# Optimization experiments

Measured on AMD Instinct MI355X. Metric: run time of the kernel, lower is better.

## Reference

```python
import jax, jax.numpy as jnp
import numpy as np

GRID = 32
N = GRID * GRID
KTOP = 256          # max off-diagonal points kept per diagram (rest are diagonal, zero cost)
SINK_ITERS = 150
_idx = np.arange(N).reshape(GRID, GRID)
_EU = np.concatenate([_idx[:, :-1].ravel(), _idx[:-1, :].ravel()]).astype(np.int32)
_EV = np.concatenate([_idx[:, 1:].ravel(), _idx[1:, :].ravel()]).astype(np.int32)
E = _EU.shape[0]  # 1984 grid edges (4-connectivity, V-construction cubical complex)


def _h0_pairs(v):
    """0-dim persistence pairs of the sublevel filtration of pixel values v [N].
    Kruskal/union-find with the elder rule; trivial edges emit diagonal (w, w) pairs."""
    eu, ev = jnp.asarray(_EU), jnp.asarray(_EV)
    w = jnp.maximum(v[eu], v[ev])
    order = jnp.argsort(w)

    @jax.checkpoint
    def step(state, edge):
        parent, birth = state
        u, vv, wgt = edge
        for _ in range(10):              # pointer jumping: full compression (2^10 >= N)
            parent = parent[parent]
        ru, rv = parent[u], parent[vv]
        bu, bv = birth[ru], birth[rv]
        merge = ru != rv
        u_older = bu <= bv
        older = jnp.where(u_older, ru, rv)
        younger = jnp.where(u_older, rv, ru)
        pb = jnp.where(merge, jnp.maximum(bu, bv), wgt)   # younger component dies
        parent = parent.at[younger].set(jnp.where(merge, older, younger))
        birth = birth.at[older].set(jnp.minimum(bu, bv))
        return (parent, birth), (pb, wgt)

    init = (jnp.arange(N, dtype=jnp.int32), v)
    _, (bs, ds) = jax.lax.scan(step, init, (eu[order], ev[order], w[order]))
    return bs, ds


def _diagrams(img):
    """img [GRID,GRID] -> (b0, d0, b1, d1), each [KTOP]. H1 via superlevel H0 duality."""
    v = img.reshape(-1)
    b0, d0 = _h0_pairs(v)
    b0 = jnp.concatenate([b0, v.min()[None]])   # essential H0 class: (min, max)
    d0 = jnp.concatenate([d0, v.max()[None]])
    nb, nd = _h0_pairs(-v)                       # superlevel-set H0 (essential dropped)
    b1, d1 = -nd, -nb

    def topk(b, d):
        _, i = jax.lax.top_k(d - b, KTOP)        # keep most persistent points
        return b[i], d[i]

    return (*topk(b0, d0), *topk(b1, d1))


def _wasserstein(ab, ad, bb, bd):
    """Entropic 1-Wasserstein between diagrams with L-inf ground metric and diagonal slots."""
    K = ab.shape[0]
    Pa = jnp.stack([ab, ad], -1)
    Pb = jnp.stack([bb, bd], -1)
    Mpp = jnp.max(jnp.abs(Pa[:, None, :] - Pb[None, :, :]), -1)  # [K,K]
    da = 0.5 * (ad - ab)                       # L-inf distance of a-points to diagonal
    db = 0.5 * (bd - bb)
    C = jnp.block([[Mpp, jnp.broadcast_to(da[:, None], (K, K))],
                   [jnp.broadcast_to(db[None, :], (K, K)), jnp.zeros((K, K), ab.dtype)]])
    eps = 0.02 * jnp.maximum(jnp.max(C), 1e-6)

    def it(_, fg):
        f, g = fg
        f = -eps * jax.nn.logsumexp((g[None, :] - C) / eps, axis=1)
        g = -eps * jax.nn.logsumexp((f[:, None] - C) / eps, axis=0)
        return f, g

    f, g = jax.lax.fori_loop(0, SINK_ITERS, it, (jnp.zeros(2 * K), jnp.zeros(2 * K)))
    P = jnp.exp((f[:, None] + g[None, :] - C) / eps)
    return jnp.sum(P * C)


def setup_inputs() -> dict:
    key = jax.random.key(0)
    kx, ky = jax.random.split(key)
    x = jax.random.normal(kx, (4, 4, 256, 256), dtype=jnp.float32)
    y = jax.random.randint(ky, (4, 1, 256, 256), 0, 4)
    return {"x": x, "y": y}


def reference(x, y):
    B, C, H, W = x.shape
    x = jax.nn.softmax(x, axis=1)                               # apply_nonlin
    y_oh = (y == jnp.arange(C)[None, :, None, None]).astype(x.dtype)  # scatter_ one-hot
    kh, kw = H // GRID, W // GRID

    def pool(t):  # adaptive_avg_pool2d to (32, 32)
        b, c = t.shape[:2]
        return t.reshape(b, c, GRID, kh, GRID, kw).mean((3, 5))

    mx = pool(x[:, 1:]).reshape(-1, GRID, GRID)  # drop background channel
    my = pool(y_oh[:, 1:]).reshape(-1, GRID, GRID)
    dx = jax.vmap(_diagrams)(mx)
    dy = jax.vmap(_diagrams)(my)
    w0 = jax.vmap(_wasserstein)(dx[0], dx[1], dy[0], dy[1])
    w1 = jax.vmap(_wasserstein)(dx[2], dx[3], dy[2], dy[3])
    return (jnp.sum(w0) + jnp.sum(w1)) / B
```

## Files before the change

kernel.cpp:

```cpp
#include <hip/hip_runtime.h>
#include <cmath>

#define NPIX 1024
#define NEDGE 1984
#define NPAD 2048
#define KTOP 256
#define NITER 150

typedef __attribute__((ext_vector_type(8))) short bf16x8_t;
typedef __attribute__((ext_vector_type(4))) float f32x4_t;

__device__ __forceinline__ unsigned bf_rne(float x) {
    unsigned b = __float_as_uint(x);
    return (b + 0x7fffu + ((b >> 16) & 1u)) >> 16;
}
__device__ __forceinline__ float rcpf(float x) { return __builtin_amdgcn_rcpf(x); }

template<int CTRL>
__device__ __forceinline__ float dppf(float x) {
    return __int_as_float(__builtin_amdgcn_update_dpp(
        __float_as_int(x), __float_as_int(x), CTRL, 0xF, 0xF, false));
}
__device__ __forceinline__ void wave_red2(float& s, float& m) {
    s += dppf<0x121>(s); m = fminf(m, dppf<0x121>(m));
    s += dppf<0x122>(s); m = fminf(m, dppf<0x122>(m));
    s += dppf<0x124>(s); m = fminf(m, dppf<0x124>(m));
    s += dppf<0x128>(s); m = fminf(m, dppf<0x128>(m));
    s += __int_as_float(__builtin_amdgcn_ds_swizzle(__float_as_int(s), 0x401F));
    m = fminf(m, __int_as_float(__builtin_amdgcn_ds_swizzle(__float_as_int(m), 0x401F)));
    float s0 = __int_as_float(__builtin_amdgcn_readlane(__float_as_int(s), 0));
    float s1 = __int_as_float(__builtin_amdgcn_readlane(__float_as_int(s), 32));
    s = s0 + s1;
    float m0 = __int_as_float(__builtin_amdgcn_readlane(__float_as_int(m), 0));
    float m1 = __int_as_float(__builtin_amdgcn_readlane(__float_as_int(m), 32));
    m = fminf(m0, m1);
}

__device__ __forceinline__ float min8v(const float* a) {
    float4 x0 = *(const float4*)a, x1 = *(const float4*)(a + 4);
    return fminf(fminf(fminf(x0.x, x0.y), fminf(x0.z, x0.w)),
                 fminf(fminf(x1.x, x1.y), fminf(x1.z, x1.w)));
}
__device__ __forceinline__ float sum8v(const float* a) {
    float4 x0 = *(const float4*)a, x1 = *(const float4*)(a + 4);
    return ((x0.x + x0.y) + (x0.z + x0.w)) + ((x1.x + x1.y) + (x1.z + x1.w));
}

__global__ __launch_bounds__(256) void pool_kernel(const float* __restrict__ x,
                                                   const int* __restrict__ y,
                                                   float* __restrict__ pooled) {
    int blk = blockIdx.x;
    int img = blk >> 2;
    int cell = ((blk & 3) << 8) | threadIdx.x;
    int gi = cell >> 5, gj = cell & 31;
    const float L2E = 1.4426950408889634f;
    float acc = 0.f;
    if (img < 12) {
        int b = img / 3, c = img % 3 + 1;
        const float* xb = x + (size_t)b * 262144 + (size_t)gi * 2048 + gj * 8;
        for (int pi = 0; pi < 8; ++pi) {
            const float* xr = xb + pi * 256;
            #pragma unroll
            for (int ph = 0; ph < 2; ++ph) {
                float4 c0 = *(const float4*)(xr + ph * 4);
                float4 c1 = *(const float4*)(xr + ph * 4 + 65536);
                float4 c2 = *(const float4*)(xr + ph * 4 + 131072);
                float4 c3 = *(const float4*)(xr + ph * 4 + 196608);
                const float* f0 = (const float*)&c0;
                const float* f1 = (const float*)&c1;
                const float* f2 = (const float*)&c2;
                const float* f3 = (const float*)&c3;
                #pragma unroll
                for (int k = 0; k < 4; ++k) {
                    float e0 = exp2f(f0[k] * L2E), e1 = exp2f(f1[k] * L2E);
                    float e2 = exp2f(f2[k] * L2E), e3 = exp2f(f3[k] * L2E);
                    float ec = (c == 1) ? e1 : (c == 2) ? e2 : e3;
                    acc += ec / (e0 + e1 + e2 + e3);
                }
            }
        }
    } else {
        int tt = img - 12;
        int b = tt / 3, c = tt % 3 + 1;
        const int* yb = y + (size_t)b * 65536 + (size_t)gi * 2048 + gj * 8;
        int cnt = 0;
        for (int pi = 0; pi < 8; ++pi) {
            const int* yr = yb + pi * 256;
            #pragma unroll
            for (int pj = 0; pj < 8; ++pj) cnt += (yr[pj] == c) ? 1 : 0;
        }
        acc = (float)cnt;
    }
    pooled[img * NPIX + cell] = acc * (1.f / 64.f);
}

__device__ void bitonic2048(unsigned long long* keys, int tid, bool asc) {
    for (int k = 2; k <= NPAD; k <<= 1) {
        for (int j = k >> 1; j > 0; j >>= 1) {
            for (int ii = tid; ii < NPAD; ii += 512) {
                int l = ii ^ j;
                if (l > ii) {
                    unsigned long long a = keys[ii], b = keys[l];
                    bool up = (((ii & k) == 0) == asc);
                    if ((a > b) == up) { keys[ii] = b; keys[l] = a; }
                }
            }
            __syncthreads();
        }
    }
}

__global__ __launch_bounds__(512) void diag_kernel(const float* __restrict__ pooled,
                                                   float* __restrict__ diag) {
    __shared__ float v_[NPIX];
    __shared__ unsigned long long keys[NPAD];
    __shared__ unsigned long long PB[NPIX];
    __shared__ unsigned euv[NPAD];
    __shared__ unsigned long long pbd[NEDGE];
    __shared__ unsigned long long snap[132];
    __shared__ float redA[8], redB[8];
    __shared__ float svmin, svmax;

    int run = blockIdx.x;
    int img = run >> 1, filt = run & 1;
    int tid = threadIdx.x;
    const float* m = pooled + img * NPIX;

    for (int i = tid; i < NPIX; i += 512) {
        float val = m[i];
        v_[i] = filt ? -val : val;
    }
    __syncthreads();
    float mn = INFINITY, mx = -INFINITY;
    for (int i = tid; i < NPIX; i += 512) { float vv = v_[i]; mn = fminf(mn, vv); mx = fmaxf(mx, vv); }
    for (int o = 32; o; o >>= 1) { mn = fminf(mn, __shfl_xor(mn, o)); mx = fmaxf(mx, __shfl_xor(mx, o)); }
    if ((tid & 63) == 0) { redA[tid >> 6] = mn; redB[tid >> 6] = mx; }
    __syncthreads();
    if (tid == 0) {
        float a = INFINITY, b = -INFINITY;
        for (int i2 = 0; i2 < 8; ++i2) { a = fminf(a, redA[i2]); b = fmaxf(b, redB[i2]); }
        svmin = a; svmax = b;
    }
    for (int e = tid; e < NPAD; e += 512) {
        unsigned long long key;
        unsigned uv = 0;
        if (e < NEDGE) {
            int u, vv;
            if (e < 992) { int r = e / 31; u = e + r; vv = u + 1; }
            else         { u = e - 992;   vv = u + 32; }
            float w = fmaxf(v_[u], v_[vv]);
            unsigned int bw = __float_as_uint(w);
            bw = (bw & 0x80000000u) ? ~bw : (bw | 0x80000000u);
            key = ((unsigned long long)bw << 11) | (unsigned int)e;
            uv = (unsigned)u | ((unsigned)vv << 16);
        } else key = ~0ULL;
        keys[e] = key;
        euv[e] = uv;
    }
    for (int i = tid; i < NPIX; i += 512)
        PB[i] = ((unsigned long long)__float_as_uint(v_[i]) << 32) | (unsigned)i;
    __syncthreads();
    bitonic2048(keys, tid, true);

    unsigned* PBlo = (unsigned*)PB;
    for (int base = 0; base < NEDGE; base += 128) {
        if (base) {
            for (int rd = 0; rd < 4; ++rd) {
                for (int i = tid; i < NPIX; i += 512) {
                    unsigned pp = PBlo[2 * i];
                    unsigned gg = PBlo[2 * pp];
                    PBlo[2 * i] = gg;
                }
            }
        }
        __syncthreads();
        int bend = (base + 128 < NEDGE) ? base + 128 : NEDGE;
        int bcnt = bend - base;
        if (tid < bcnt) {
            int kk = base + tid;
            unsigned long long key = keys[kk];
            int e = (int)(key & 2047ULL);
            unsigned bw = (unsigned)(key >> 11);
            unsigned uv = euv[e];
            int ra = (int)(uv & 0xffffu), rb = (int)(uv >> 16);
            unsigned pp = PBlo[2 * ra];
            while (pp != (unsigned)ra) { ra = (int)pp; pp = PBlo[2 * ra]; }
            unsigned p2 = PBlo[2 * rb];
            while (p2 != (unsigned)rb) { rb = (int)p2; p2 = PBlo[2 * rb]; }
            if (ra == rb) {
                unsigned wb = (bw & 0x80000000u) ? (bw & 0x7fffffffu) : ~bw;
                pbd[kk] = (unsigned long long)wb | ((unsigned long long)wb << 32);
                snap[tid] = (unsigned long long)bw << 22;
            } else {
                snap[tid] = ((unsigned long long)bw << 22)
                          | ((unsigned)(ra + 1) << 11) | (unsigned)(rb + 1);
            }
        }
        __syncthreads();
        if (tid == 0) {
            unsigned long long sc = snap[0];
            for (int i = 0; i < bcnt; ++i) {
                unsigned long long sn = snap[i + 1];
                if ((unsigned)(sc & 0x3FFFFFu)) {
                    unsigned ob = (unsigned)(sc >> 22);
                    float w = __uint_as_float((ob & 0x80000000u) ? (ob & 0x7fffffffu) : ~ob);
                    int a = (int)((sc >> 11) & 0x7FFu) - 1;
                    int b = (int)(sc & 0x7FFu) - 1;
                    unsigned long long qa = PB[a], qb = PB[b];
                    int pa = (int)(unsigned)qa, pb = (int)(unsigned)qb;
                    while (pa != a || pb != b) {
                        if (pa != a) {
                            unsigned long long na = PB[pa];
                            int ga = (int)(unsigned)na;
                            PBlo[2 * a] = (unsigned)ga;
                            a = pa; pa = ga; qa = na;
                        }
                        if (pb != b) {
                            unsigned long long nb = PB[pb];
                            int gb = (int)(unsigned)nb;
                            PBlo[2 * b] = (unsigned)gb;
                            b = pb; pb = gb; qb = nb;
                        }
                    }
                    float pb_, pd_;
                    if (a != b) {
                        float bu = __uint_as_float((unsigned)(qa >> 32));
                        float bv = __uint_as_float((unsigned)(qb >> 32));
                        bool uo = (bu <= bv);
                        int older = uo ? a : b;
                        int younger = uo ? b : a;
                        pb_ = fmaxf(bu, bv); pd_ = w;
                        PBlo[2 * younger] = (unsigned)older;
                    } else { pb_ = w; pd_ = w; }
                    pbd[base + i] = (unsigned long long)__float_as_uint(pb_)
                                  | ((unsigned long long)__float_as_uint(pd_) << 32);
                }
                sc = sn;
            }
        }
        __syncthreads();
    }

    int count = filt ? NEDGE : (NEDGE + 1);
    for (int k = tid; k < NPAD; k += 512) {
        unsigned long long key = 0ULL;
        if (k < count) {
            float pers;
            if (k < NEDGE) {
                unsigned long long pd2 = pbd[k];
                pers = __uint_as_float((unsigned)(pd2 >> 32)) - __uint_as_float((unsigned)pd2);
            } else pers = svmax - svmin;
            key = ((unsigned long long)__float_as_uint(pers) << 32) | (unsigned int)(2047 - k);
        }
        keys[k] = key;
    }
    __syncthreads();
    bitonic2048(keys, tid, false);

    if (tid < KTOP) {
        unsigned long long key = keys[tid];
        int k = 2047 - (int)(key & 0xffffffffULL);
        float b_, d_;
        if (k < NEDGE) {
            unsigned long long pd2 = pbd[k];
            b_ = __uint_as_float((unsigned)pd2);
            d_ = __uint_as_float((unsigned)(pd2 >> 32));
        } else { b_ = svmin; d_ = svmax; }
        float ob, od;
        if (!filt) { ob = b_;  od = d_;  }
        else       { ob = -d_; od = -b_; }
        diag[((img * 4) + filt * 2 + 0) * KTOP + tid] = ob;
        diag[((img * 4) + filt * 2 + 1) * KTOP + tid] = od;
    }
}

__global__ __launch_bounds__(512) void sink_kernel(const float* __restrict__ diag,
                                                   float* __restrict__ wres) {
    __shared__ float2 sPA[KTOP], sPB[KTOP];
    __shared__ float sda[KTOP], sdb[KTOP];
    __shared__ float swa[KTOP], swb[KTOP];
    __shared__ __align__(16) unsigned ug_bf[128];
    __shared__ __align__(16) unsigned uf_bf[128];
    __shared__ __align__(16) float uf32[KTOP], ug32[KTOP];
    __shared__ __align__(16) float minF[8], accTF[8], minG[8], accTG[8];
    __shared__ __align__(16) float pm[8];
    __shared__ float s_sig, s_invsig;

    int p = blockIdx.x;
    int img = p % 12, dim = p / 12;
    int t = threadIdx.x;
    int lane = t & 63, w = t >> 6;
    int lr = lane & 15, lg = lane >> 4;
    int r = t >> 1, q = t & 1, jb = q * 128;

    const float* ab  = diag + ((img * 4) + dim * 2) * KTOP;
    const float* ad  = ab + KTOP;
    const float* bbp = diag + (((12 + img) * 4) + dim * 2) * KTOP;
    const float* bdp = bbp + KTOP;

    if (t < KTOP) {
        float a0 = ab[t], a1 = ad[t];
        float b0 = bbp[t], b1 = bdp[t];
        sPA[t] = make_float2(a0, a1);
        sPB[t] = make_float2(b0, b1);
        sda[t] = 0.5f * (a1 - a0);
        sdb[t] = 0.5f * (b1 - b0);
    }
    if (t < 128) ug_bf[t] = 0x3F803F80u;
    __syncthreads();

    {
        float2 A = sPA[r];
        float lmax = 0.f;
        for (int jj = 0; jj < 128; ++jj) {
            float2 B = sPB[jb + jj];
            lmax = fmaxf(lmax, fmaxf(fabsf(A.x - B.x), fabsf(A.y - B.y)));
        }
        if (t < KTOP) lmax = fmaxf(lmax, fmaxf(sda[t], sdb[t]));
        for (int o = 32; o; o >>= 1) lmax = fmaxf(lmax, __shfl_xor(lmax, o));
        if (lane == 0) pm[w] = lmax;
    }
    __syncthreads();
    if (t == 0) {
        float mc = 0.f;
        for (int i = 0; i < 8; ++i) mc = fmaxf(mc, pm[i]);
        float eps = 0.02f * fmaxf(mc, 1e-6f);
        s_sig = 1.4426950408889634f / eps;
        s_invsig = eps * 0.6931471805599453f;
    }
    __syncthreads();
    {
        float sig = s_sig;
        if (t < KTOP) {
            float2 a2 = sPA[t], b2 = sPB[t];
            sPA[t] = make_float2(a2.x * sig, a2.y * sig);
            sPB[t] = make_float2(b2.x * sig, b2.y * sig);
            float da2 = sda[t] * sig, db2 = sdb[t] * sig;
            sda[t] = da2; sdb[t] = db2;
            swa[t] = exp2f(-da2); swb[t] = exp2f(-db2);
        }
    }
    __syncthreads();

    bf16x8_t KfA0[8], KfA1[8], KgA0[8], KgA1[8];
    {
        float2 Af0 = sPA[w * 32 + lr];
        float2 Af1 = sPA[w * 32 + 16 + lr];
        float2 Bg0 = sPB[w * 32 + lr];
        float2 Bg1 = sPB[w * 32 + 16 + lr];
        #pragma unroll
        for (int ks = 0; ks < 8; ++ks) {
            #pragma unroll
            for (int jj = 0; jj < 8; ++jj) {
                int b = ks * 32 + lg * 8 + jj;
                float2 Pb = sPB[b];
                KfA0[ks][jj] = (short)bf_rne(exp2f(-fmaxf(fabsf(Af0.x - Pb.x), fabsf(Af0.y - Pb.y))));
                KfA1[ks][jj] = (short)bf_rne(exp2f(-fmaxf(fabsf(Af1.x - Pb.x), fabsf(Af1.y - Pb.y))));
                float2 Pa = sPA[b];
                KgA0[ks][jj] = (short)bf_rne(exp2f(-fmaxf(fabsf(Pa.x - Bg0.x), fabsf(Pa.y - Bg0.y))));
                KgA1[ks][jj] = (short)bf_rne(exp2f(-fmaxf(fabsf(Pa.x - Bg1.x), fabsf(Pa.y - Bg1.y))));
            }
        }
    }
    float wa0[4], wa1[4], wb0[4], wb1[4];
    #pragma unroll
    for (int g2 = 0; g2 < 4; ++g2) {
        wa0[g2] = swa[w * 32 + lg * 4 + g2];
        wa1[g2] = swa[w * 32 + 16 + lg * 4 + g2];
        wb0[g2] = swb[w * 32 + lg * 4 + g2];
        wb1[g2] = swb[w * 32 + 16 + lg * 4 + g2];
    }

    float cg = 1.f, cf = 1.f, uG2s = 1.f, uF2s = 1.f;
    f32x4_t ugs0 = {1.f, 1.f, 1.f, 1.f}, ugs1 = {1.f, 1.f, 1.f, 1.f};
    f32x4_t ufs0 = {0.f, 0.f, 0.f, 0.f}, ufs1 = {0.f, 0.f, 0.f, 0.f};

    for (int it = 0; it < NITER; ++it) {
        if (it) {
            cg = min8v(minG);
            uG2s = rcpf(cf * (sum8v(accTG) + 256.f * uF2s));
        }
        {
            bf16x8_t Bf[8];
            #pragma unroll
            for (int ks = 0; ks < 8; ++ks) Bf[ks] = ((const bf16x8_t*)ug_bf)[ks * 4 + lg];
            f32x4_t a0 = {0.f, 0.f, 0.f, 0.f}, a1 = {0.f, 0.f, 0.f, 0.f};
            #pragma unroll
            for (int ks = 0; ks < 8; ++ks) {
                a0 = __builtin_amdgcn_mfma_f32_16x16x32_bf16(KfA0[ks], Bf[ks], a0, 0, 0, 0);
                a1 = __builtin_amdgcn_mfma_f32_16x16x32_bf16(KfA1[ks], Bf[ks], a1, 0, 0, 0);
            }
            float mv = INFINITY, tv = 0.f;
            #pragma unroll
            for (int g2 = 0; g2 < 4; ++g2) {
                float R0 = cg * (a0[g2] + 256.f * uG2s * wa0[g2]);
                float R1 = cg * (a1[g2] + 256.f * uG2s * wa1[g2]);
                ufs0[g2] = rcpf(R0); ufs1[g2] = rcpf(R1);
                mv = fminf(mv, fminf(R0, R1));
                tv += ugs0[g2] * wb0[g2] + ugs1[g2] * wb1[g2];
            }
            if (lr == 0) {
                uint2 v0, v1;
                v0.x = bf_rne(ufs0[0]) | (bf_rne(ufs0[1]) << 16);
                v0.y = bf_rne(ufs0[2]) | (bf_rne(ufs0[3]) << 16);
                v1.x = bf_rne(ufs1[0]) | (bf_rne(ufs1[1]) << 16);
                v1.y = bf_rne(ufs1[2]) | (bf_rne(ufs1[3]) << 16);
                ((uint2*)uf_bf)[w * 8 + lg] = v0;
                ((uint2*)uf_bf)[w * 8 + 4 + lg] = v1;
            }
            wave_red2(tv, mv);
            if (lane == 0) { accTF[w] = tv * 0.0625f; minF[w] = mv; }
        }
        __syncthreads();
        cf = min8v(minF);
        uF2s = rcpf(cg * (sum8v(accTF) + 256.f * uG2s));
        {
            bf16x8_t Bf[8];
            #pragma unroll
            for (int ks = 0; ks < 8; ++ks) Bf[ks] = ((const bf16x8_t*)uf_bf)[ks * 4 + lg];
            f32x4_t a0 = {0.f, 0.f, 0.f, 0.f}, a1 = {0.f, 0.f, 0.f, 0.f};
            #pragma unroll
            for (int ks = 0; ks < 8; ++ks) {
                a0 = __builtin_amdgcn_mfma_f32_16x16x32_bf16(KgA0[ks], Bf[ks], a0, 0, 0, 0);
                a1 = __builtin_amdgcn_mfma_f32_16x16x32_bf16(KgA1[ks], Bf[ks], a1, 0, 0, 0);
            }
            float mv = INFINITY, tv = 0.f;
            #pragma unroll
            for (int g2 = 0; g2 < 4; ++g2) {
                float Q0 = cf * (a0[g2] + 256.f * uF2s * wb0[g2]);
                float Q1 = cf * (a1[g2] + 256.f * uF2s * wb1[g2]);
                ugs0[g2] = rcpf(Q0); ugs1[g2] = rcpf(Q1);
                mv = fminf(mv, fminf(Q0, Q1));
                tv += ufs0[g2] * wa0[g2] + ufs1[g2] * wa1[g2];
            }
            if (lr == 0) {
                uint2 v0, v1;
                v0.x = bf_rne(ugs0[0]) | (bf_rne(ugs0[1]) << 16);
                v0.y = bf_rne(ugs0[2]) | (bf_rne(ugs0[3]) << 16);
                v1.x = bf_rne(ugs1[0]) | (bf_rne(ugs1[1]) << 16);
                v1.y = bf_rne(ugs1[2]) | (bf_rne(ugs1[3]) << 16);
                ((uint2*)ug_bf)[w * 8 + lg] = v0;
                ((uint2*)ug_bf)[w * 8 + 4 + lg] = v1;
            }
            wave_red2(tv, mv);
            if (lane == 0) { accTG[w] = tv * 0.0625f; minG[w] = mv; }
        }
        __syncthreads();
    }
    float uG2f = rcpf(cf * (sum8v(accTG) + 256.f * uF2s));
    if (lr == 0) {
        ((f32x4_t*)uf32)[w * 8 + lg] = ufs0;
        ((f32x4_t*)uf32)[w * 8 + 4 + lg] = ufs1;
        ((f32x4_t*)ug32)[w * 8 + lg] = ugs0;
        ((f32x4_t*)ug32)[w * 8 + 4 + lg] = ugs1;
    }
    __syncthreads();

    float accv = 0.f;
    {
        float2 Apt = sPA[r];
        float ufr = uf32[r];
        #pragma unroll 8
        for (int jj = 0; jj < 128; ++jj) {
            int j = jb + jj;
            float2 B = sPB[j];
            float Mh = fmaxf(fabsf(Apt.x - B.x), fabsf(Apt.y - B.y));
            float kv = __uint_as_float(bf_rne(exp2f(-Mh)) << 16);
            accv += ((ufr * kv) * ug32[j]) * Mh;
        }
        if (q == 0) accv += 256.f * ((ufr * swa[r]) * uG2f) * sda[r];
        else        accv += 256.f * ((uF2s * swb[r]) * ug32[r]) * sdb[r];
    }
    accv *= cf;
    for (int o = 32; o; o >>= 1) accv += __shfl_xor(accv, o);
    if (lane == 0) pm[w] = accv;
    __syncthreads();
    if (t == 0) {
        float tot = 0.f;
        for (int i = 0; i < 8; ++i) tot += pm[i];
        wres[p] = tot * s_invsig;
    }
}

__global__ void finalize_kernel(const float* __restrict__ wres, float* __restrict__ out) {
    if (threadIdx.x == 0) {
        float s = 0.f;
        for (int i = 0; i < 24; ++i) s += wres[i];
        out[0] = s * 0.25f;
    }
}

extern "C" void kernel_launch(void* const* d_in, const int* in_sizes, int n_in,
                              void* d_out, int out_size, void* d_ws, size_t ws_size,
                              hipStream_t stream) {
    const float* x = (const float*)d_in[0];
    const int* y = (const int*)d_in[1];
    float* ws = (float*)d_ws;
    float* pooled = ws;
    float* diag = pooled + 24 * NPIX;
    float* wres = diag + 24 * 4 * KTOP;

    pool_kernel<<<96, 256, 0, stream>>>(x, y, pooled);
    diag_kernel<<<48, 512, 0, stream>>>(pooled, diag);
    sink_kernel<<<24, 512, 0, stream>>>(diag, wres);
    finalize_kernel<<<1, 64, 0, stream>>>(wres, (float*)d_out);
}
```

Before: 892.9 us.

## Replace top-k bitonic sort with radix select and register-local bitonic tail

Replaces the second full 2048-element bitonic sort, used only to pick the 256 most persistent pairs, with an 8-round byte-wise radix select that finds the threshold key, then compacts matching entries through an atomic counter. Output order becomes arbitrary, which the Wasserstein stage should tolerate since it treats points as a set. The remaining edge sort handles its last two merge stages per stage in registers, four elements per thread, which removes barriers for j<4. Ties at zero keys (key != 0 filter) and nondeterministic order add some risk.

```diff
diff --git a/kernel.cpp b/kernel.cpp
--- a/kernel.cpp
+++ b/kernel.cpp
@@ -94,10 +94,16 @@
     pooled[img * NPIX + cell] = acc * (1.f / 64.f);
 }
 
-__device__ void bitonic2048(unsigned long long* keys, int tid, bool asc) {
+__device__ __forceinline__ void cex(unsigned long long& a, unsigned long long& b, bool up) {
+    if ((a > b) == up) { unsigned long long t = a; a = b; b = t; }
+}
+__device__ void bitonic2048_reg(unsigned long long* keys, int tid, bool asc) {
+    int i0 = tid << 2;
     for (int k = 2; k <= NPAD; k <<= 1) {
-        for (int j = k >> 1; j > 0; j >>= 1) {
-            for (int ii = tid; ii < NPAD; ii += 512) {
+        for (int j = k >> 1; j >= 4; j >>= 1) {
+            #pragma unroll
+            for (int rep = 0; rep < 4; ++rep) {
+                int ii = tid + rep * 512;
                 int l = ii ^ j;
                 if (l > ii) {
                     unsigned long long a = keys[ii], b = keys[l];
@@ -107,6 +113,17 @@
             }
             __syncthreads();
         }
+        unsigned long long e0 = keys[i0], e1 = keys[i0 + 1], e2 = keys[i0 + 2], e3 = keys[i0 + 3];
+        bool upq = (((i0 & k) == 0) == asc);
+        if (k >= 4) {
+            cex(e0, e2, upq); cex(e1, e3, upq);
+            cex(e0, e1, upq); cex(e2, e3, upq);
+        } else {
+            cex(e0, e1, asc);
+            cex(e2, e3, !asc);
+        }
+        keys[i0] = e0; keys[i0 + 1] = e1; keys[i0 + 2] = e2; keys[i0 + 3] = e3;
+        __syncthreads();
     }
 }
 
@@ -118,12 +135,16 @@
     __shared__ unsigned euv[NPAD];
     __shared__ unsigned long long pbd[NEDGE];
     __shared__ unsigned long long snap[132];
+    __shared__ unsigned histAll[2048];
     __shared__ float redA[8], redB[8];
     __shared__ float svmin, svmax;
+    __shared__ unsigned long long s_prefix, s_T;
+    __shared__ unsigned s_need, s_done, s_outcnt;
 
     int run = blockIdx.x;
     int img = run >> 1, filt = run & 1;
     int tid = threadIdx.x;
+    int wv = tid >> 6;
     const float* m = pooled + img * NPIX;
 
     for (int i = tid; i < NPIX; i += 512) {
@@ -134,7 +155,7 @@
     float mn = INFINITY, mx = -INFINITY;
     for (int i = tid; i < NPIX; i += 512) { float vv = v_[i]; mn = fminf(mn, vv); mx = fmaxf(mx, vv); }
     for (int o = 32; o; o >>= 1) { mn = fminf(mn, __shfl_xor(mn, o)); mx = fmaxf(mx, __shfl_xor(mx, o)); }
-    if ((tid & 63) == 0) { redA[tid >> 6] = mn; redB[tid >> 6] = mx; }
+    if ((tid & 63) == 0) { redA[wv] = mn; redB[wv] = mx; }
     __syncthreads();
     if (tid == 0) {
         float a = INFINITY, b = -INFINITY;
@@ -160,7 +181,7 @@
     for (int i = tid; i < NPIX; i += 512)
         PB[i] = ((unsigned long long)__float_as_uint(v_[i]) << 32) | (unsigned)i;
     __syncthreads();
-    bitonic2048(keys, tid, true);
+    bitonic2048_reg(keys, tid, true);
 
     unsigned* PBlo = (unsigned*)PB;
     for (int base = 0; base < NEDGE; base += 128) {
@@ -254,23 +275,80 @@
         }
         keys[k] = key;
     }
-    __syncthreads();
-    bitonic2048(keys, tid, false);
-
-    if (tid < KTOP) {
-        unsigned long long key = keys[tid];
-        int k = 2047 - (int)(key & 0xffffffffULL);
-        float b_, d_;
-        if (k < NEDGE) {
-            unsigned long long pd2 = pbd[k];
-            b_ = __uint_as_float((unsigned)pd2);
-            d_ = __uint_as_float((unsigned)(pd2 >> 32));
-        } else { b_ = svmin; d_ = svmax; }
-        float ob, od;
-        if (!filt) { ob = b_;  od = d_;  }
-        else       { ob = -d_; od = -b_; }
-        diag[((img * 4) + filt * 2 + 0) * KTOP + tid] = ob;
-        diag[((img * 4) + filt * 2 + 1) * KTOP + tid] = od;
+    if (tid == 0) { s_prefix = 0ULL; s_T = 0ULL; s_need = KTOP; s_done = 0; s_outcnt = 0; }
+    __syncthreads();
+
+    for (int rnd = 0; rnd < 8; ++rnd) {
+        for (int i = tid; i < 2048; i += 512) histAll[i] = 0;
+        __syncthreads();
+        if (!s_done) {
+            int shift = 56 - 8 * rnd;
+            unsigned long long pref = s_prefix;
+            for (int k = tid; k < NPAD; k += 512) {
+                unsigned long long key = keys[k];
+                bool act = (rnd == 0) || ((key >> (shift + 8)) == (pref >> (shift + 8)));
+                if (act) atomicAdd(&histAll[wv * 256 + (unsigned)((key >> shift) & 255ULL)], 1u);
+            }
+        }
+        __syncthreads();
+        if (wv == 0) {
+            if (!s_done) {
+                int l64 = tid;
+                int shift = 56 - 8 * rnd;
+                unsigned c0 = 0, c1 = 0, c2 = 0, c3 = 0;
+                #pragma unroll
+                for (int cp = 0; cp < 8; ++cp) {
+                    const unsigned* h = histAll + cp * 256 + 4 * l64;
+                    c0 += h[0]; c1 += h[1]; c2 += h[2]; c3 += h[3];
+                }
+                unsigned s3 = c3, s2 = c2 + s3, s1 = c1 + s2, s0 = c0 + s1;
+                unsigned acc2 = s0;
+                #pragma unroll
+                for (int o = 1; o < 64; o <<= 1) {
+                    unsigned v2 = __shfl_down(acc2, o);
+                    if (l64 + o < 64) acc2 += v2;
+                }
+                unsigned above = acc2 - s0;
+                unsigned Sn[5] = {above + s0, above + s1, above + s2, above + s3, above};
+                unsigned need = s_need;
+                #pragma unroll
+                for (int q2 = 0; q2 < 4; ++q2) {
+                    if (Sn[q2] >= need && Sn[q2 + 1] < need) {
+                        unsigned bstar = 4 * l64 + q2;
+                        if (Sn[q2] == need) {
+                            s_T = s_prefix | ((unsigned long long)bstar << shift);
+                            s_done = 1;
+                        } else {
+                            s_prefix = s_prefix | ((unsigned long long)bstar << shift);
+                            s_need = need - Sn[q2 + 1];
+                        }
+                    }
+                }
+            }
+        }
+        __syncthreads();
+    }
+
+    {
+        unsigned long long T = s_T;
+        for (int k = tid; k < NPAD; k += 512) {
+            unsigned long long key = keys[k];
+            if (key >= T && key != 0ULL) {
+                int pos = (int)atomicAdd(&s_outcnt, 1u);
+                int kk = 2047 - (int)(key & 0xffffffffULL);
+                float b_, d_;
+                if (kk < NEDGE) {
+                    unsigned long long pd2 = pbd[kk];
+                    b_ = __uint_as_float((unsigned)pd2);
+                    d_ = __uint_as_float((unsigned)(pd2 >> 32));
+                } else { b_ = svmin; d_ = svmax; }
+                float ob, od;
+                if (!filt) { ob = b_;  od = d_;  }
+                else       { ob = -d_; od = -b_; }
+                diag[((img * 4) + filt * 2 + 0) * KTOP + pos] = ob;
+                diag[((img * 4) + filt * 2 + 1) * KTOP + pos] = od;
+            }
+        }
     }
 }
 
```

New measurement: 834.9 us. 6.5% less time.
